# Kernel tuning notes

Hardware: AMD Instinct MI355X
Metric: run time of the kernel (lower is better)

The kernel has to match this reference:

```python
import jax, jax.numpy as jnp
import numpy as np

SEQ_LEN = 512
HID = 2048
VOCAB = 128
OUT = 2


def setup_inputs() -> dict:
    key = jax.random.key(0)
    ks = jax.random.split(key, 7)
    s = 1.0 / np.sqrt(HID)
    return {
        "inputs": jax.random.randint(ks[0], (SEQ_LEN,), 0, VOCAB),
        "hx": jnp.zeros((1, HID), jnp.float32),
        "emb": jax.random.normal(ks[1], (VOCAB, HID), jnp.float32) * s,
        "w_ih": jax.random.normal(ks[2], (3 * HID, HID), jnp.float32) * s,
        "w_hh": jax.random.normal(ks[3], (3 * HID, HID), jnp.float32) * s,
        "b_ih": jax.random.normal(ks[4], (3 * HID,), jnp.float32) * s,
        "b_hh": jax.random.normal(ks[5], (3 * HID,), jnp.float32) * s,
        "w_out": jax.random.normal(ks[6], (OUT, HID), jnp.float32) * s,
        "b_out": jnp.zeros((OUT,), jnp.float32),
    }


def reference(inputs, hx, emb, w_ih, w_hh, b_ih, b_hh, w_out, b_out):
    # embed: [L] -> [L, 1, H] (batch of 1, matching view(len, 1, -1))
    x = emb[inputs][:, None, :]

    def gru_step(h, xt):
        gi = xt @ w_ih.T + b_ih            # [1, 3H]
        gh = h @ w_hh.T + b_hh             # [1, 3H]
        i_r, i_z, i_n = jnp.split(gi, 3, axis=-1)
        h_r, h_z, h_n = jnp.split(gh, 3, axis=-1)
        r = jax.nn.sigmoid(i_r + h_r)
        z = jax.nn.sigmoid(i_z + h_z)
        n = jnp.tanh(i_n + r * h_n)
        h_new = (1.0 - z) * n + z * h
        return h_new, None

    h_final, _ = jax.lax.scan(gru_step, hx, x)
    logits = h_final @ w_out.T + b_out     # [1, OUT]
    return jax.nn.log_softmax(logits, axis=1)
```

## Files before the change

kernel.cpp:

```cpp
#include <hip/hip_runtime.h>

#define HID    2048
#define G3     6144
#define NVOCAB 128
#define SEQ    512
#define NBLK   256
#define TAGBASE 0x5EED0000u

__device__ __forceinline__ float sigmoidf_(float x) {
  return 1.f / (1.f + __expf(-x));
}
__device__ __forceinline__ float tanhf_(float x) {
  const float ax = fabsf(x);
  const float e2 = __expf(-2.f * ax);
  return copysignf((1.f - e2) / (1.f + e2), x);
}

__global__ __launch_bounds__(256) void gi_precompute(
    const float* __restrict__ emb,
    const float* __restrict__ w_ih,
    const float* __restrict__ b_ih,
    float* __restrict__ GI) {
  __shared__ float sE[64][33];
  __shared__ float sW[64][33];

  const int j0 = blockIdx.x * 64;
  const int v0 = blockIdx.y * 64;
  const int tid = threadIdx.x;
  const int tx = tid & 15;
  const int ty = tid >> 4;
  const int r  = tid >> 3;
  const int c4 = (tid & 7) * 4;

  float acc[4][4] = {};

  for (int k0 = 0; k0 < HID; k0 += 32) {
    __syncthreads();
    float4 eA = *(const float4*)&emb [(size_t)(v0 + r)      * HID + k0 + c4];
    float4 eB = *(const float4*)&emb [(size_t)(v0 + r + 32) * HID + k0 + c4];
    float4 wA = *(const float4*)&w_ih[(size_t)(j0 + r)      * HID + k0 + c4];
    float4 wB = *(const float4*)&w_ih[(size_t)(j0 + r + 32) * HID + k0 + c4];
    sE[r][c4+0] = eA.x; sE[r][c4+1] = eA.y; sE[r][c4+2] = eA.z; sE[r][c4+3] = eA.w;
    sE[r+32][c4+0] = eB.x; sE[r+32][c4+1] = eB.y; sE[r+32][c4+2] = eB.z; sE[r+32][c4+3] = eB.w;
    sW[r][c4+0] = wA.x; sW[r][c4+1] = wA.y; sW[r][c4+2] = wA.z; sW[r][c4+3] = wA.w;
    sW[r+32][c4+0] = wB.x; sW[r+32][c4+1] = wB.y; sW[r+32][c4+2] = wB.z; sW[r+32][c4+3] = wB.w;
    __syncthreads();

    #pragma unroll
    for (int kk = 0; kk < 32; ++kk) {
      float e0 = sE[ty*4+0][kk], e1 = sE[ty*4+1][kk];
      float e2 = sE[ty*4+2][kk], e3 = sE[ty*4+3][kk];
      float w0 = sW[tx*4+0][kk], w1 = sW[tx*4+1][kk];
      float w2 = sW[tx*4+2][kk], w3 = sW[tx*4+3][kk];
      acc[0][0] += e0*w0; acc[0][1] += e0*w1; acc[0][2] += e0*w2; acc[0][3] += e0*w3;
      acc[1][0] += e1*w0; acc[1][1] += e1*w1; acc[1][2] += e1*w2; acc[1][3] += e1*w3;
      acc[2][0] += e2*w0; acc[2][1] += e2*w1; acc[2][2] += e2*w2; acc[2][3] += e2*w3;
      acc[3][0] += e3*w0; acc[3][1] += e3*w1; acc[3][2] += e3*w2; acc[3][3] += e3*w3;
    }
  }

  #pragma unroll
  for (int a = 0; a < 4; ++a)
    #pragma unroll
    for (int b = 0; b < 4; ++b) {
      const int j = j0 + tx*4 + b;
      GI[(size_t)(v0 + ty*4 + a) * G3 + j] = acc[a][b] + b_ih[j];
    }
}

__global__ __launch_bounds__(256, 1) void gru_reg(
    const float* __restrict__ GI,
    const float* __restrict__ Whh,
    const float* __restrict__ bhh,
    const int*   __restrict__ inputs,
    const float* __restrict__ wout,
    const float* __restrict__ bout,
    unsigned long long* __restrict__ bufU,
    unsigned* __restrict__ done,
    float* __restrict__ out,
    const float* __restrict__ hx) {

  __shared__ int   s_inp[SEQ];
  __shared__ float s_h[HID];
  __shared__ float s_logits[2];

  const int tid  = threadIdx.x;
  const int lane = tid & 63;
  const int wv   = tid >> 6;
  const int i0 = blockIdx.x * 4 + wv;
  const int i1 = i0 + 1024;
  unsigned* flag0 = done + 256 * 16;

  for (int k = tid; k < SEQ; k += 256) s_inp[k] = inputs[k];

  float w_r0[32], w_z0[32], w_n0[32], w_r1[32], w_z1[32], w_n1[32];
  {
    const float* pr0 = Whh + (size_t)i0 * HID;
    const float* pz0 = Whh + (size_t)(i0 + HID) * HID;
    const float* pn0 = Whh + (size_t)(i0 + 2*HID) * HID;
    const float* pr1 = Whh + (size_t)i1 * HID;
    const float* pz1 = Whh + (size_t)(i1 + HID) * HID;
    const float* pn1 = Whh + (size_t)(i1 + 2*HID) * HID;
    #pragma unroll
    for (int c = 0; c < 8; ++c) {
      const int k = c * 256 + lane * 4;
      *(float4*)&w_r0[c*4] = *(const float4*)&pr0[k];
      *(float4*)&w_z0[c*4] = *(const float4*)&pz0[k];
      *(float4*)&w_n0[c*4] = *(const float4*)&pn0[k];
      *(float4*)&w_r1[c*4] = *(const float4*)&pr1[k];
      *(float4*)&w_z1[c*4] = *(const float4*)&pz1[k];
      *(float4*)&w_n1[c*4] = *(const float4*)&pn1[k];
    }
  }
  #pragma unroll
  for (int c = 0; c < 32; ++c) {
    asm volatile("" : "+a"(w_r0[c]), "+a"(w_z0[c]), "+a"(w_n0[c]),
                      "+a"(w_r1[c]), "+a"(w_z1[c]), "+a"(w_n1[c]));
  }

  const float br0 = bhh[i0], bz0 = bhh[i0+HID], bn0 = bhh[i0+2*HID];
  const float br1 = bhh[i1], bz1 = bhh[i1+HID], bn1 = bhh[i1+2*HID];

  __syncthreads();

  float g0r, g0z, g0n, g1r, g1z, g1n;
  {
    const float* gp = GI + (size_t)s_inp[0] * G3;
    g0r = gp[i0]; g0z = gp[i0+HID]; g0n = gp[i0+2*HID];
    g1r = gp[i1]; g1z = gp[i1+HID]; g1n = gp[i1+2*HID];
  }

  for (int s = 0; s < SEQ; ++s) {
    if (s == 0) {
      #pragma unroll
      for (int j = 0; j < 8; ++j) s_h[j*256 + tid] = hx[j*256 + tid];
    } else {
      const unsigned wantTag = TAGBASE | (unsigned)s;
      const unsigned long long* br_ = bufU + (size_t)(s & 1) * HID;
      unsigned pending = 0xFFu;
      while (pending) {
        unsigned long long x[8];
        #pragma unroll
        for (int j = 0; j < 8; ++j)
          if (pending & (1u << j))
            x[j] = __hip_atomic_load(br_ + j*256 + tid, __ATOMIC_RELAXED,
                                     __HIP_MEMORY_SCOPE_AGENT);
        #pragma unroll
        for (int j = 0; j < 8; ++j)
          if ((pending & (1u << j)) && (unsigned)(x[j] >> 32) == wantTag) {
            s_h[j*256 + tid] = __uint_as_float((unsigned)x[j]);
            pending &= ~(1u << j);
          }
      }
    }
    __syncthreads();

    float ng0r=g0r, ng0z=g0z, ng0n=g0n, ng1r=g1r, ng1z=g1z, ng1n=g1n;
    if (s + 1 < SEQ) {
      const float* gp = GI + (size_t)s_inp[s+1] * G3;
      ng0r = gp[i0]; ng0z = gp[i0+HID]; ng0n = gp[i0+2*HID];
      ng1r = gp[i1]; ng1z = gp[i1+HID]; ng1n = gp[i1+2*HID];
    }

    float ar0=0.f, az0=0.f, an0=0.f, ar1=0.f, az1=0.f, an1=0.f;
    #pragma unroll
    for (int c = 0; c < 8; ++c) {
      const float4 h4 = *(const float4*)&s_h[c*256 + lane*4];
      ar0 = fmaf(w_r0[c*4+0], h4.x, ar0); ar0 = fmaf(w_r0[c*4+1], h4.y, ar0);
      ar0 = fmaf(w_r0[c*4+2], h4.z, ar0); ar0 = fmaf(w_r0[c*4+3], h4.w, ar0);
      az0 = fmaf(w_z0[c*4+0], h4.x, az0); az0 = fmaf(w_z0[c*4+1], h4.y, az0);
      az0 = fmaf(w_z0[c*4+2], h4.z, az0); az0 = fmaf(w_z0[c*4+3], h4.w, az0);
      an0 = fmaf(w_n0[c*4+0], h4.x, an0); an0 = fmaf(w_n0[c*4+1], h4.y, an0);
      an0 = fmaf(w_n0[c*4+2], h4.z, an0); an0 = fmaf(w_n0[c*4+3], h4.w, an0);
      ar1 = fmaf(w_r1[c*4+0], h4.x, ar1); ar1 = fmaf(w_r1[c*4+1], h4.y, ar1);
      ar1 = fmaf(w_r1[c*4+2], h4.z, ar1); ar1 = fmaf(w_r1[c*4+3], h4.w, ar1);
      az1 = fmaf(w_z1[c*4+0], h4.x, az1); az1 = fmaf(w_z1[c*4+1], h4.y, az1);
      az1 = fmaf(w_z1[c*4+2], h4.z, az1); az1 = fmaf(w_z1[c*4+3], h4.w, az1);
      an1 = fmaf(w_n1[c*4+0], h4.x, an1); an1 = fmaf(w_n1[c*4+1], h4.y, an1);
      an1 = fmaf(w_n1[c*4+2], h4.z, an1); an1 = fmaf(w_n1[c*4+3], h4.w, an1);
    }

    const float hp0 = s_h[i0], hp1 = s_h[i1];

    #pragma unroll
    for (int m = 32; m > 0; m >>= 1) {
      ar0 += __shfl_xor(ar0, m); az0 += __shfl_xor(az0, m); an0 += __shfl_xor(an0, m);
      ar1 += __shfl_xor(ar1, m); az1 += __shfl_xor(az1, m); an1 += __shfl_xor(an1, m);
    }

    if (lane == 0) {
      const unsigned tagv = TAGBASE | (unsigned)(s + 1);
      unsigned long long* bw = bufU + (size_t)((s + 1) & 1) * HID;
      const float r0 = sigmoidf_(g0r + ar0 + br0);
      const float z0 = sigmoidf_(g0z + az0 + bz0);
      const float n0 = tanhf_(g0n + r0 * (an0 + bn0));
      const float h0n = (1.f - z0) * n0 + z0 * hp0;
      const float r1 = sigmoidf_(g1r + ar1 + br1);
      const float z1 = sigmoidf_(g1z + az1 + bz1);
      const float n1 = tanhf_(g1n + r1 * (an1 + bn1));
      const float h1n = (1.f - z1) * n1 + z1 * hp1;
      __hip_atomic_store(bw + i0,
          ((unsigned long long)tagv << 32) | (unsigned long long)__float_as_uint(h0n),
          __ATOMIC_RELAXED, __HIP_MEMORY_SCOPE_AGENT);
      __hip_atomic_store(bw + i1,
          ((unsigned long long)tagv << 32) | (unsigned long long)__float_as_uint(h1n),
          __ATOMIC_RELAXED, __HIP_MEMORY_SCOPE_AGENT);
    }

    g0r = ng0r; g0z = ng0z; g0n = ng0n;
    g1r = ng1r; g1z = ng1z; g1n = ng1n;

    __syncthreads();
  }

  if (blockIdx.x == 0) {
    {
      const unsigned wantTag = TAGBASE | (unsigned)SEQ;
      const unsigned long long* br_ = bufU;
      unsigned pending = 0xFFu;
      while (pending) {
        unsigned long long x[8];
        #pragma unroll
        for (int j = 0; j < 8; ++j)
          if (pending & (1u << j))
            x[j] = __hip_atomic_load(br_ + j*256 + tid, __ATOMIC_RELAXED,
                                     __HIP_MEMORY_SCOPE_AGENT);
        #pragma unroll
        for (int j = 0; j < 8; ++j)
          if ((pending & (1u << j)) && (unsigned)(x[j] >> 32) == wantTag) {
            s_h[j*256 + tid] = __uint_as_float((unsigned)x[j]);
            pending &= ~(1u << j);
          }
      }
    }
    __syncthreads();
    if (tid == 0)
      __hip_atomic_store(flag0, 0xD0D0D0D0u, __ATOMIC_RELAXED,
                         __HIP_MEMORY_SCOPE_AGENT);

    if (wv < 2) {
      const float* wo = wout + (size_t)wv * HID;
      float acc = 0.f;
      #pragma unroll
      for (int c = 0; c < 8; ++c) {
        const float4 h4 = *(const float4*)&s_h[c*256 + lane*4];
        const float4 a4 = *(const float4*)&wo[c*256 + lane*4];
        acc += a4.x*h4.x + a4.y*h4.y + a4.z*h4.z + a4.w*h4.w;
      }
      #pragma unroll
      for (int m = 32; m > 0; m >>= 1) acc += __shfl_xor(acc, m);
      if (lane == 0) s_logits[wv] = acc + bout[wv];
    }
    __syncthreads();
    if (tid == 0) {
      const float l0 = s_logits[0], l1 = s_logits[1];
      const float mx = fmaxf(l0, l1);
      const float lse = mx + logf(expf(l0 - mx) + expf(l1 - mx));
      out[0] = l0 - lse;
      out[1] = l1 - lse;
    }
    if (tid < 8) {
      const int slot = (tid & 3) + (tid >> 2) * 1024;
      __hip_atomic_store(bufU + slot, 0ull, __ATOMIC_RELAXED, __HIP_MEMORY_SCOPE_AGENT);
      __hip_atomic_store(bufU + HID + slot, 0ull, __ATOMIC_RELAXED, __HIP_MEMORY_SCOPE_AGENT);
    }
    if (tid >= 1) {
      while (__hip_atomic_load(done + tid * 16, __ATOMIC_RELAXED,
                               __HIP_MEMORY_SCOPE_AGENT) != 0xD1D1D1D1u)
        __builtin_amdgcn_s_sleep(8);
    }
    __syncthreads();
    __hip_atomic_store(done + tid * 16, 0u, __ATOMIC_RELAXED, __HIP_MEMORY_SCOPE_AGENT);
    if (tid == 0)
      __hip_atomic_store(flag0, 0u, __ATOMIC_RELAXED, __HIP_MEMORY_SCOPE_AGENT);
  } else {
    if (tid == 0) {
      while (__hip_atomic_load(flag0, __ATOMIC_RELAXED,
                               __HIP_MEMORY_SCOPE_AGENT) != 0xD0D0D0D0u)
        __builtin_amdgcn_s_sleep(8);
    }
    __syncthreads();
    if (tid < 8) {
      const int slot = blockIdx.x * 4 + (tid & 3) + (tid >> 2) * 1024;
      __hip_atomic_store(bufU + slot, 0ull, __ATOMIC_RELAXED, __HIP_MEMORY_SCOPE_AGENT);
      __hip_atomic_store(bufU + HID + slot, 0ull, __ATOMIC_RELAXED, __HIP_MEMORY_SCOPE_AGENT);
    }
    asm volatile("s_waitcnt vmcnt(0)" ::: "memory");
    __syncthreads();
    if (tid == 0)
      __hip_atomic_store(done + blockIdx.x * 16, 0xD1D1D1D1u, __ATOMIC_RELAXED,
                         __HIP_MEMORY_SCOPE_AGENT);
  }
}

__global__ __launch_bounds__(256) void gru_step_fb(
    const float* __restrict__ GI,
    const float* __restrict__ Whh,
    const float* __restrict__ bhh,
    const int*   __restrict__ inputs, int t,
    const float* __restrict__ h_in,
    float* __restrict__ h_out) {
  const int lane = threadIdx.x & 63;
  const int wvv  = threadIdx.x >> 6;
  const int i = blockIdx.x * 4 + wvv;
  const int v = inputs[t];

  const float4* hv = (const float4*)h_in;
  const float4* wr = (const float4*)(Whh + (size_t)i*HID);
  const float4* wz = (const float4*)(Whh + (size_t)(i+HID)*HID);
  const float4* wn = (const float4*)(Whh + (size_t)(i+2*HID)*HID);

  float ar=0.f, az=0.f, an=0.f;
  #pragma unroll
  for (int c = 0; c < 8; ++c) {
    const int idx = c*64 + lane;
    const float4 h4 = hv[idx];
    float4 a;
    a = wr[idx]; ar += a.x*h4.x + a.y*h4.y + a.z*h4.z + a.w*h4.w;
    a = wz[idx]; az += a.x*h4.x + a.y*h4.y + a.z*h4.z + a.w*h4.w;
    a = wn[idx]; an += a.x*h4.x + a.y*h4.y + a.z*h4.z + a.w*h4.w;
  }
  #pragma unroll
  for (int m = 32; m > 0; m >>= 1) {
    ar += __shfl_xor(ar, m); az += __shfl_xor(az, m); an += __shfl_xor(an, m);
  }
  if (lane == 0) {
    const float* gi = GI + (size_t)v * G3;
    const float r = sigmoidf_(gi[i] + ar + bhh[i]);
    const float z = sigmoidf_(gi[i+HID] + az + bhh[i+HID]);
    const float n = tanhf_(gi[i+2*HID] + r * (an + bhh[i+2*HID]));
    h_out[i] = (1.f - z) * n + z * h_in[i];
  }
}

__global__ void gru_out_fb(const float* __restrict__ h,
                           const float* __restrict__ wout,
                           const float* __restrict__ bout,
                           float* out) {
  __shared__ float logits[2];
  const int lane = threadIdx.x & 63;
  const int wvv  = threadIdx.x >> 6;
  if (wvv < 2) {
    const float4* wo = (const float4*)(wout + (size_t)wvv * HID);
    const float4* hv = (const float4*)h;
    float acc = 0.f;
    #pragma unroll
    for (int c = 0; c < 8; ++c) {
      const int idx = c*64 + lane;
      const float4 a  = wo[idx];
      const float4 h4 = hv[idx];
      acc += a.x*h4.x + a.y*h4.y + a.z*h4.z + a.w*h4.w;
    }
    #pragma unroll
    for (int m = 32; m > 0; m >>= 1) acc += __shfl_xor(acc, m);
    if (lane == 0) logits[wvv] = acc + bout[wvv];
  }
  __syncthreads();
  if (threadIdx.x == 0) {
    const float l0 = logits[0], l1 = logits[1];
    const float mx = fmaxf(l0, l1);
    const float lse = mx + logf(expf(l0 - mx) + expf(l1 - mx));
    out[0] = l0 - lse;
    out[1] = l1 - lse;
  }
}

extern "C" void kernel_launch(void* const* d_in, const int* in_sizes, int n_in,
                              void* d_out, int out_size, void* d_ws, size_t ws_size,
                              hipStream_t stream) {
  const int*   inputs = (const int*)  d_in[0];
  const float* hx     = (const float*)d_in[1];
  const float* emb    = (const float*)d_in[2];
  const float* w_ih   = (const float*)d_in[3];
  const float* w_hh   = (const float*)d_in[4];
  const float* b_ih   = (const float*)d_in[5];
  const float* b_hh   = (const float*)d_in[6];
  const float* w_out  = (const float*)d_in[7];
  const float* b_out  = (const float*)d_in[8];
  float* out = (float*)d_out;

  float* GI = (float*)d_ws;
  unsigned long long* bufU =
      (unsigned long long*)((char*)d_ws + (size_t)NVOCAB * G3 * 4);
  unsigned* done = (unsigned*)(bufU + 2 * HID);

  gi_precompute<<<dim3(G3/64, NVOCAB/64), 256, 0, stream>>>(emb, w_ih, b_ih, GI);

  void* args[] = { (void*)&GI, (void*)&w_hh, (void*)&b_hh, (void*)&inputs,
                   (void*)&w_out, (void*)&b_out, (void*)&bufU, (void*)&done,
                   (void*)&out, (void*)&hx };
  hipError_t ce = hipLaunchCooperativeKernel((void*)gru_reg, dim3(NBLK), dim3(256),
                                             args, 0, stream);
  if (ce != hipSuccess) {
    float* h0 = (float*)bufU;
    float* h1 = h0 + HID;
    const float* hin = hx;
    for (int t = 0; t < SEQ; ++t) {
      float* hout = (t & 1) ? h1 : h0;
      gru_step_fb<<<512, 256, 0, stream>>>(GI, w_hh, b_hh, inputs, t, hin, hout);
      hin = hout;
    }
    gru_out_fb<<<1, 128, 0, stream>>>(hin, w_out, b_out, out);
  }
}
```

Measured before the change: 2.239 ms.

## Halve persistent GRU blocks, give each wave four hidden units, stagger polling

The persistent recurrent kernel moves from 256 to 128 blocks. Each wave now holds weight rows for four hidden units (12 rows in AGPR/VGPR registers), and four lanes compute the gate outputs in parallel instead of lane 0 computing them all. The polling loop for the shared hidden state now rotates its start address per block and adds a short sleep between retries, to spread contention on the exchange buffer. This cuts the number of blocks that must synchronise each step, at the cost of more per-wave FMA work and higher register pressure (384 weight registers per lane).

```diff
diff --git a/kernel.cpp b/kernel.cpp
--- a/kernel.cpp
+++ b/kernel.cpp
@@ -4,7 +4,7 @@
 #define G3     6144
 #define NVOCAB 128
 #define SEQ    512
-#define NBLK   256
+#define NBLK   128
 #define TAGBASE 0x5EED0000u
 
 __device__ __forceinline__ float sigmoidf_(float x) {
@@ -87,47 +87,53 @@
   const int tid  = threadIdx.x;
   const int lane = tid & 63;
   const int wv   = tid >> 6;
-  const int i0 = blockIdx.x * 4 + wv;
-  const int i1 = i0 + 1024;
-  unsigned* flag0 = done + 256 * 16;
+  const int wid  = blockIdx.x * 4 + wv;
+  const int rot  = (blockIdx.x << 3);
+  unsigned* flag0 = done + NBLK * 16;
 
   for (int k = tid; k < SEQ; k += 256) s_inp[k] = inputs[k];
 
-  float w_r0[32], w_z0[32], w_n0[32], w_r1[32], w_z1[32], w_n1[32];
+  float wR0[32], wR1[32], wR2[32], wR3[32];
+  float wZ0[32], wZ1[32], wZ2[32], wZ3[32];
+  float wN0[32], wN1[32], wN2[32], wN3[32];
   {
-    const float* pr0 = Whh + (size_t)i0 * HID;
-    const float* pz0 = Whh + (size_t)(i0 + HID) * HID;
-    const float* pn0 = Whh + (size_t)(i0 + 2*HID) * HID;
-    const float* pr1 = Whh + (size_t)i1 * HID;
-    const float* pz1 = Whh + (size_t)(i1 + HID) * HID;
-    const float* pn1 = Whh + (size_t)(i1 + 2*HID) * HID;
-    #pragma unroll
-    for (int c = 0; c < 8; ++c) {
-      const int k = c * 256 + lane * 4;
-      *(float4*)&w_r0[c*4] = *(const float4*)&pr0[k];
-      *(float4*)&w_z0[c*4] = *(const float4*)&pz0[k];
-      *(float4*)&w_n0[c*4] = *(const float4*)&pn0[k];
-      *(float4*)&w_r1[c*4] = *(const float4*)&pr1[k];
-      *(float4*)&w_z1[c*4] = *(const float4*)&pz1[k];
-      *(float4*)&w_n1[c*4] = *(const float4*)&pn1[k];
+    #pragma unroll
+    for (int q = 0; q < 4; ++q) {
+      const int u = wid + (q << 9);
+      const float* pr = Whh + (size_t)u * HID;
+      const float* pz = Whh + (size_t)(u + HID) * HID;
+      const float* pn = Whh + (size_t)(u + 2*HID) * HID;
+      float* dr = q==0 ? wR0 : q==1 ? wR1 : q==2 ? wR2 : wR3;
+      float* dz = q==0 ? wZ0 : q==1 ? wZ1 : q==2 ? wZ2 : wZ3;
+      float* dn = q==0 ? wN0 : q==1 ? wN1 : q==2 ? wN2 : wN3;
+      #pragma unroll
+      for (int c = 0; c < 8; ++c) {
+        const int k = c * 256 + lane * 4;
+        *(float4*)&dr[c*4] = *(const float4*)&pr[k];
+        *(float4*)&dz[c*4] = *(const float4*)&pz[k];
+        *(float4*)&dn[c*4] = *(const float4*)&pn[k];
+      }
     }
   }
   #pragma unroll
   for (int c = 0; c < 32; ++c) {
-    asm volatile("" : "+a"(w_r0[c]), "+a"(w_z0[c]), "+a"(w_n0[c]),
-                      "+a"(w_r1[c]), "+a"(w_z1[c]), "+a"(w_n1[c]));
-  }
-
-  const float br0 = bhh[i0], bz0 = bhh[i0+HID], bn0 = bhh[i0+2*HID];
-  const float br1 = bhh[i1], bz1 = bhh[i1+HID], bn1 = bhh[i1+2*HID];
+    asm volatile("" : "+a"(wR0[c]), "+a"(wR1[c]), "+a"(wR2[c]), "+a"(wR3[c]),
+                      "+a"(wZ0[c]), "+a"(wZ1[c]), "+a"(wZ2[c]), "+a"(wZ3[c]),
+                      "+v"(wN0[c]), "+v"(wN1[c]), "+v"(wN2[c]), "+v"(wN3[c]));
+  }
+
+  const int q  = lane & 3;
+  const int uq = wid + (q << 9);
+  const float b_r = bhh[uq];
+  const float b_z = bhh[uq + HID];
+  const float b_n = bhh[uq + 2*HID];
 
   __syncthreads();
 
-  float g0r, g0z, g0n, g1r, g1z, g1n;
+  float g_r, g_z, g_n;
   {
     const float* gp = GI + (size_t)s_inp[0] * G3;
-    g0r = gp[i0]; g0z = gp[i0+HID]; g0n = gp[i0+2*HID];
-    g1r = gp[i1]; g1z = gp[i1+HID]; g1n = gp[i1+2*HID];
+    g_r = gp[uq]; g_z = gp[uq + HID]; g_n = gp[uq + 2*HID];
   }
 
   for (int s = 0; s < SEQ; ++s) {
@@ -138,77 +144,79 @@
       const unsigned wantTag = TAGBASE | (unsigned)s;
       const unsigned long long* br_ = bufU + (size_t)(s & 1) * HID;
       unsigned pending = 0xFFu;
+      bool first = true;
       while (pending) {
+        if (!first) __builtin_amdgcn_s_sleep(1);
+        first = false;
         unsigned long long x[8];
         #pragma unroll
         for (int j = 0; j < 8; ++j)
           if (pending & (1u << j))
-            x[j] = __hip_atomic_load(br_ + j*256 + tid, __ATOMIC_RELAXED,
-                                     __HIP_MEMORY_SCOPE_AGENT);
+            x[j] = __hip_atomic_load(br_ + ((j*256 + tid + rot) & (HID-1)),
+                                     __ATOMIC_RELAXED, __HIP_MEMORY_SCOPE_AGENT);
         #pragma unroll
         for (int j = 0; j < 8; ++j)
           if ((pending & (1u << j)) && (unsigned)(x[j] >> 32) == wantTag) {
-            s_h[j*256 + tid] = __uint_as_float((unsigned)x[j]);
+            s_h[(j*256 + tid + rot) & (HID-1)] = __uint_as_float((unsigned)x[j]);
             pending &= ~(1u << j);
           }
       }
     }
     __syncthreads();
 
-    float ng0r=g0r, ng0z=g0z, ng0n=g0n, ng1r=g1r, ng1z=g1z, ng1n=g1n;
+    float ng_r = g_r, ng_z = g_z, ng_n = g_n;
     if (s + 1 < SEQ) {
       const float* gp = GI + (size_t)s_inp[s+1] * G3;
-      ng0r = gp[i0]; ng0z = gp[i0+HID]; ng0n = gp[i0+2*HID];
-      ng1r = gp[i1]; ng1z = gp[i1+HID]; ng1n = gp[i1+2*HID];
-    }
-
-    float ar0=0.f, az0=0.f, an0=0.f, ar1=0.f, az1=0.f, an1=0.f;
+      ng_r = gp[uq]; ng_z = gp[uq + HID]; ng_n = gp[uq + 2*HID];
+    }
+
+    float r0=0.f,r1=0.f,r2=0.f,r3=0.f;
+    float z0=0.f,z1=0.f,z2=0.f,z3=0.f;
+    float n0=0.f,n1=0.f,n2=0.f,n3=0.f;
     #pragma unroll
     for (int c = 0; c < 8; ++c) {
       const float4 h4 = *(const float4*)&s_h[c*256 + lane*4];
-      ar0 = fmaf(w_r0[c*4+0], h4.x, ar0); ar0 = fmaf(w_r0[c*4+1], h4.y, ar0);
-      ar0 = fmaf(w_r0[c*4+2], h4.z, ar0); ar0 = fmaf(w_r0[c*4+3], h4.w, ar0);
-      az0 = fmaf(w_z0[c*4+0], h4.x, az0); az0 = fmaf(w_z0[c*4+1], h4.y, az0);
-      az0 = fmaf(w_z0[c*4+2], h4.z, az0); az0 = fmaf(w_z0[c*4+3], h4.w, az0);
-      an0 = fmaf(w_n0[c*4+0], h4.x, an0); an0 = fmaf(w_n0[c*4+1], h4.y, an0);
-      an0 = fmaf(w_n0[c*4+2], h4.z, an0); an0 = fmaf(w_n0[c*4+3], h4.w, an0);
-      ar1 = fmaf(w_r1[c*4+0], h4.x, ar1); ar1 = fmaf(w_r1[c*4+1], h4.y, ar1);
-      ar1 = fmaf(w_r1[c*4+2], h4.z, ar1); ar1 = fmaf(w_r1[c*4+3], h4.w, ar1);
-      az1 = fmaf(w_z1[c*4+0], h4.x, az1); az1 = fmaf(w_z1[c*4+1], h4.y, az1);
-      az1 = fmaf(w_z1[c*4+2], h4.z, az1); az1 = fmaf(w_z1[c*4+3], h4.w, az1);
-      an1 = fmaf(w_n1[c*4+0], h4.x, an1); an1 = fmaf(w_n1[c*4+1], h4.y, an1);
-      an1 = fmaf(w_n1[c*4+2], h4.z, an1); an1 = fmaf(w_n1[c*4+3], h4.w, an1);
-    }
-
-    const float hp0 = s_h[i0], hp1 = s_h[i1];
+      #pragma unroll
+      for (int e = 0; e < 4; ++e) {
+        const float hv = e==0 ? h4.x : e==1 ? h4.y : e==2 ? h4.z : h4.w;
+        const int k = c*4 + e;
+        r0 = fmaf(wR0[k], hv, r0); r1 = fmaf(wR1[k], hv, r1);
+        r2 = fmaf(wR2[k], hv, r2); r3 = fmaf(wR3[k], hv, r3);
+        z0 = fmaf(wZ0[k], hv, z0); z1 = fmaf(wZ1[k], hv, z1);
+        z2 = fmaf(wZ2[k], hv, z2); z3 = fmaf(wZ3[k], hv, z3);
+        n0 = fmaf(wN0[k], hv, n0); n1 = fmaf(wN1[k], hv, n1);
+        n2 = fmaf(wN2[k], hv, n2); n3 = fmaf(wN3[k], hv, n3);
+      }
+    }
+
+    const float hp = s_h[uq];
 
     #pragma unroll
     for (int m = 32; m > 0; m >>= 1) {
-      ar0 += __shfl_xor(ar0, m); az0 += __shfl_xor(az0, m); an0 += __shfl_xor(an0, m);
-      ar1 += __shfl_xor(ar1, m); az1 += __shfl_xor(az1, m); an1 += __shfl_xor(an1, m);
-    }
-
-    if (lane == 0) {
+      r0 += __shfl_xor(r0, m); r1 += __shfl_xor(r1, m);
+      r2 += __shfl_xor(r2, m); r3 += __shfl_xor(r3, m);
+      z0 += __shfl_xor(z0, m); z1 += __shfl_xor(z1, m);
+      z2 += __shfl_xor(z2, m); z3 += __shfl_xor(z3, m);
+      n0 += __shfl_xor(n0, m); n1 += __shfl_xor(n1, m);
+      n2 += __shfl_xor(n2, m); n3 += __shfl_xor(n3, m);
+    }
+
+    const float ar = q==0 ? r0 : q==1 ? r1 : q==2 ? r2 : r3;
+    const float az = q==0 ? z0 : q==1 ? z1 : q==2 ? z2 : z3;
+    const float an = q==0 ? n0 : q==1 ? n1 : q==2 ? n2 : n3;
+    const float rg = sigmoidf_(g_r + ar + b_r);
+    const float zg = sigmoidf_(g_z + az + b_z);
+    const float ng = tanhf_(g_n + rg * (an + b_n));
+    const float hnew = (1.f - zg) * ng + zg * hp;
+    if (lane < 4) {
+      unsigned long long* bw = bufU + (size_t)((s + 1) & 1) * HID;
       const unsigned tagv = TAGBASE | (unsigned)(s + 1);
-      unsigned long long* bw = bufU + (size_t)((s + 1) & 1) * HID;
-      const float r0 = sigmoidf_(g0r + ar0 + br0);
-      const float z0 = sigmoidf_(g0z + az0 + bz0);
-      const float n0 = tanhf_(g0n + r0 * (an0 + bn0));
-      const float h0n = (1.f - z0) * n0 + z0 * hp0;
-      const float r1 = sigmoidf_(g1r + ar1 + br1);
-      const float z1 = sigmoidf_(g1z + az1 + bz1);
-      const float n1 = tanhf_(g1n + r1 * (an1 + bn1));
-      const float h1n = (1.f - z1) * n1 + z1 * hp1;
-      __hip_atomic_store(bw + i0,
-          ((unsigned long long)tagv << 32) | (unsigned long long)__float_as_uint(h0n),
+      __hip_atomic_store(bw + uq,
+          ((unsigned long long)tagv << 32) | (unsigned long long)__float_as_uint(hnew),
           __ATOMIC_RELAXED, __HIP_MEMORY_SCOPE_AGENT);
-      __hip_atomic_store(bw + i1,
-          ((unsigned long long)tagv << 32) | (unsigned long long)__float_as_uint(h1n),
-          __ATOMIC_RELAXED, __HIP_MEMORY_SCOPE_AGENT);
-    }
-
-    g0r = ng0r; g0z = ng0z; g0n = ng0n;
-    g1r = ng1r; g1z = ng1z; g1n = ng1n;
+    }
+
+    g_r = ng_r; g_z = ng_z; g_n = ng_n;
 
     __syncthreads();
   }
@@ -259,18 +267,19 @@
       out[0] = l0 - lse;
       out[1] = l1 - lse;
     }
-    if (tid < 8) {
-      const int slot = (tid & 3) + (tid >> 2) * 1024;
+    if (tid < 16) {
+      const int slot = (tid & 3) + ((tid >> 2) << 9);
       __hip_atomic_store(bufU + slot, 0ull, __ATOMIC_RELAXED, __HIP_MEMORY_SCOPE_AGENT);
       __hip_atomic_store(bufU + HID + slot, 0ull, __ATOMIC_RELAXED, __HIP_MEMORY_SCOPE_AGENT);
     }
-    if (tid >= 1) {
+    if (tid >= 1 && tid < NBLK) {
       while (__hip_atomic_load(done + tid * 16, __ATOMIC_RELAXED,
                                __HIP_MEMORY_SCOPE_AGENT) != 0xD1D1D1D1u)
         __builtin_amdgcn_s_sleep(8);
     }
     __syncthreads();
-    __hip_atomic_store(done + tid * 16, 0u, __ATOMIC_RELAXED, __HIP_MEMORY_SCOPE_AGENT);
+    if (tid < NBLK)
+      __hip_atomic_store(done + tid * 16, 0u, __ATOMIC_RELAXED, __HIP_MEMORY_SCOPE_AGENT);
     if (tid == 0)
       __hip_atomic_store(flag0, 0u, __ATOMIC_RELAXED, __HIP_MEMORY_SCOPE_AGENT);
   } else {
@@ -280,8 +289,8 @@
         __builtin_amdgcn_s_sleep(8);
     }
     __syncthreads();
-    if (tid < 8) {
-      const int slot = blockIdx.x * 4 + (tid & 3) + (tid >> 2) * 1024;
+    if (tid < 16) {
+      const int slot = blockIdx.x * 4 + (tid & 3) + ((tid >> 2) << 9);
       __hip_atomic_store(bufU + slot, 0ull, __ATOMIC_RELAXED, __HIP_MEMORY_SCOPE_AGENT);
       __hip_atomic_store(bufU + HID + slot, 0ull, __ATOMIC_RELAXED, __HIP_MEMORY_SCOPE_AGENT);
     }
```

Result: slower. 3.400 ms (+51.9%).
